# Kernel tuning notes

Hardware: AMD Instinct MI355X
Metric: run time of the kernel (lower is better)

Reference implementation:

```python
import jax, jax.numpy as jnp
import numpy as np

N = 8192
D = 512  # token_length
EPS = 1e-12  # torch F.normalize default eps


def setup_inputs() -> dict:
    key = jax.random.key(0)
    ks = jax.random.split(key, 7)
    scale = 1.0 / np.sqrt(D)  # torch Linear init range ~ U(-1/sqrt(D), 1/sqrt(D))
    def lin(k):
        kw, kb = jax.random.split(k)
        W = jax.random.uniform(kw, (D, D), jnp.float32, -scale, scale)
        b = jax.random.uniform(kb, (D,), jnp.float32, -scale, scale)
        return W, b
    Wq, bq = lin(ks[0])
    Wk, bk = lin(ks[1])
    Wv, bv = lin(ks[2])
    x = jax.random.normal(ks[3], (N, D), jnp.float32)
    return {"x": x, "Wq": Wq, "bq": bq, "Wk": Wk, "bk": bk, "Wv": Wv, "bv": bv}


def reference(x, Wq, bq, Wk, bk, Wv, bv):
    # torch Linear: y = x @ W^T + b
    q = x @ Wq.T + bq            # [N, D]
    k = x @ Wk.T + bk            # [N, D]
    v = x @ Wv.T + bv            # [N, D]
    s = q @ k.T                  # [N, N] scores
    # F.normalize(s): L2-normalize each row (dim=1), eps=1e-12
    norm = jnp.sqrt(jnp.sum(s * s, axis=1, keepdims=True))
    w = s / jnp.maximum(norm, EPS)
    return w @ v                 # [N, D]
```

## Files before the change

### kernel.cpp

```cpp
#include <hip/hip_runtime.h>
#include <hip/hip_bf16.h>
#include <stdint.h>

#define NTOK 8192
#define DIM  512
#define QKVW 1536

typedef __attribute__((ext_vector_type(8))) short bf16x8;
typedef __attribute__((ext_vector_type(4))) float f32x4;

static __device__ __forceinline__ unsigned short f2b(float f) {
    union { float f; unsigned int u; } v; v.f = f;
    unsigned int r = v.u + 0x7fffu + ((v.u >> 16) & 1u);
    return (unsigned short)(r >> 16);
}

static __device__ __forceinline__ float b2f(unsigned short u) {
    union { unsigned int i; float f; } v; v.i = ((unsigned int)u) << 16;
    return v.f;
}

static __device__ __forceinline__ void gld_lds16(const void* g, void* l) {
    __builtin_amdgcn_global_load_lds(
        (__attribute__((address_space(1))) void*)(uintptr_t)g,
        (__attribute__((address_space(3))) void*)(uintptr_t)l,
        16, 0, 0);
}

#define SBAR() do { __builtin_amdgcn_sched_barrier(0); __builtin_amdgcn_s_barrier(); __builtin_amdgcn_sched_barrier(0); } while (0)
#define VMW0() do { __builtin_amdgcn_sched_barrier(0); asm volatile("s_waitcnt vmcnt(0)" ::: "memory"); __builtin_amdgcn_sched_barrier(0); } while (0)
#define LGKM0() do { __builtin_amdgcn_sched_barrier(0); asm volatile("s_waitcnt lgkmcnt(0)" ::: "memory"); __builtin_amdgcn_sched_barrier(0); } while (0)


__global__ void f2b_kernel(const float* __restrict__ src, unsigned short* __restrict__ dst, int n4) {
    int i = blockIdx.x * blockDim.x + threadIdx.x;
    if (i < n4) {
        float4 f = ((const float4*)src)[i];
        ushort4 o;
        o.x = f2b(f.x); o.y = f2b(f.y); o.z = f2b(f.z); o.w = f2b(f.w);
        ((ushort4*)dst)[i] = o;
    }
}

__global__ void f2b_w3(const float* __restrict__ w0, const float* __restrict__ w1,
                       const float* __restrict__ w2, unsigned short* __restrict__ dst) {
    int which = blockIdx.y;
    const float* src = (which == 0) ? w0 : (which == 1) ? w1 : w2;
    int i = blockIdx.x * 256 + threadIdx.x;
    float4 f = ((const float4*)src)[i];
    ushort4 o;
    o.x = f2b(f.x); o.y = f2b(f.y); o.z = f2b(f.z); o.w = f2b(f.w);
    ((ushort4*)(dst + (size_t)which * 262144))[i] = o;
}

__global__ void bias_concat(const float* __restrict__ bq, const float* __restrict__ bk,
                            const float* __restrict__ bv, float* __restrict__ bc) {
    int i = blockIdx.x * blockDim.x + threadIdx.x;
    if (i < 512)       bc[i] = bq[i];
    else if (i < 1024) bc[i] = bk[i - 512];
    else if (i < 1536) bc[i] = bv[i - 1024];
}

template <int CH, int NT>
__global__ __launch_bounds__(256, 4) void gemm_qkv2(
    const unsigned short* __restrict__ A, int lda,
    const unsigned short* __restrict__ B, int ldb,
    unsigned short* __restrict__ Qb,
    unsigned short* __restrict__ KVt,
    const float* __restrict__ bias) {

    __shared__ __align__(16) char lds[32768];

    const int t = threadIdx.x;
    const int l = t & 63, w = t >> 6;
    const int wr = w >> 1, wc = w & 1;

    const int gx = gridDim.x;
    const int nbm = gridDim.y >> 3;
    const int bid = blockIdx.y * gx + blockIdx.x;
    const int xcd = bid & 7, qq = bid >> 3;
    const int win = nbm * CH;
    const int grp = qq / win, rr = qq % win;
    const int bm = xcd * nbm + rr / CH;
    const int bn = grp * CH + rr % CH;

    const int c0 = w * 128 + l;
    const int c1 = c0 + 64;
    const int r0 = c0 >> 2, r1 = c1 >> 2;
    const int col0 = (((c0 & 3) ^ ((c0 >> 3) & 3)) << 3);
    const int col1 = (((c1 & 3) ^ ((c1 >> 3) & 3)) << 3);
    const unsigned short* gA0 = A + (size_t)(bm * 128 + r0) * lda + col0;
    const unsigned short* gA1 = A + (size_t)(bm * 128 + r1) * lda + col1;
    const unsigned short* gB0 = B + (size_t)(bn * 128 + r0) * ldb + col0;
    const unsigned short* gB1 = B + (size_t)(bn * 128 + r1) * ldb + col1;

    auto STAGE = [&](int buf, int tt) {
        char* d = lds + buf * 16384 + w * 2048;
        const int o = tt * 32;
        gld_lds16(gA0 + o, d);
        gld_lds16(gA1 + o, d + 1024);
        gld_lds16(gB0 + o, d + 8192);
        gld_lds16(gB1 + o, d + 8192 + 1024);
    };

    f32x4 acc[4][4] = {};

    const int lr = l & 15, Q = l >> 4;
    const int sw = ((Q ^ ((lr >> 1) & 3)) << 4);
    const int lrA = (wr * 64 + lr) * 64 + sw;
    const int lrB = 8192 + (wc * 64 + lr) * 64 + sw;

    STAGE(0, 0);
    VMW0();
    SBAR();

    #pragma unroll
    for (int tt = 0; tt < NT; ++tt) {
        const int cur = tt & 1;
        const bool more = (tt + 1 < NT);
        if (more) STAGE(cur ^ 1, tt + 1);
        __builtin_amdgcn_sched_barrier(0);

        const char* lb = lds + cur * 16384;
        bf16x8 af[4], bf[4];
        #pragma unroll
        for (int m = 0; m < 4; ++m) af[m] = *(const bf16x8*)(lb + lrA + m * 1024);
        #pragma unroll
        for (int n = 0; n < 4; ++n) bf[n] = *(const bf16x8*)(lb + lrB + n * 1024);

        __builtin_amdgcn_s_setprio(1);
        #pragma unroll
        for (int m = 0; m < 4; ++m)
            #pragma unroll
            for (int n = 0; n < 4; ++n)
                acc[m][n] = __builtin_amdgcn_mfma_f32_16x16x32_bf16(af[m], bf[n], acc[m][n], 0, 0, 0);
        __builtin_amdgcn_s_setprio(0);

        if (more) {
            VMW0();
            SBAR();
        }
    }

    const int rbase = bm * 128 + wr * 64;
    const int cbase = bn * 128 + wc * 64;
    const int g4 = Q * 4;

    if (bn < 4) {
        #pragma unroll
        for (int m = 0; m < 4; ++m)
            #pragma unroll
            for (int n = 0; n < 4; ++n)
                #pragma unroll
                for (int j = 0; j < 4; ++j) {
                    int rrow = rbase + m * 16 + g4 + j;
                    int ccol = cbase + n * 16 + lr;
                    Qb[(size_t)rrow * 512 + ccol] = f2b(acc[m][n][j] + bias[ccol]);
                }
    } else {
        SBAR();
        unsigned short* wt = (unsigned short*)(lds + w * 8192);
        #pragma unroll
        for (int p = 0; p < 2; ++p) {
            #pragma unroll
            for (int m = 0; m < 4; ++m)
                #pragma unroll
                for (int q2 = 0; q2 < 2; ++q2) {
                    int n = 2 * p + q2;
                    int cloc = q2 * 16 + lr;
                    int ccol = cbase + n * 16 + lr;
                    unsigned short s0 = f2b(acc[m][n][0] + bias[ccol]);
                    unsigned short s1 = f2b(acc[m][n][1] + bias[ccol]);
                    unsigned short s2 = f2b(acc[m][n][2] + bias[ccol]);
                    unsigned short s3 = f2b(acc[m][n][3] + bias[ccol]);
                    uint2 v;
                    v.x = (unsigned int)s0 | ((unsigned int)s1 << 16);
                    v.y = (unsigned int)s2 | ((unsigned int)s3 << 16);
                    *(uint2*)(wt + cloc * 72 + m * 16 + g4) = v;
                }
            LGKM0();
            const int kvb = cbase - 512 + 32 * p;
            #pragma unroll
            for (int cc = 0; cc < 8; ++cc) {
                int cloc = cc * 4 + Q;
                uint2 v = *(const uint2*)(wt + cloc * 72 + lr * 4);
                *(uint2*)&KVt[(size_t)(kvb + cloc) * NTOK + rbase + lr * 4] = v;
            }
            if (p == 0) LGKM0();
        }
    }
}

template <int EPI, int CH, int NT>
__global__ __launch_bounds__(256, 4) void gemm7(
    const unsigned short* __restrict__ A, int lda,
    const unsigned short* __restrict__ B, int ldb,
    void* __restrict__ Cout, int ldc,
    const unsigned short* __restrict__ Qb,
    float* __restrict__ nrm) {

    __shared__ __align__(16) char lds[32768];

    const int t = threadIdx.x;
    const int l = t & 63, w = t >> 6;
    const int wr = w >> 1, wc = w & 1;

    int bm, bn;
    if constexpr (CH == 0) {
        bm = blockIdx.y; bn = blockIdx.x;
    } else {
        const int gx = gridDim.x;
        const int nbm = gridDim.y >> 3;
        const int bid = blockIdx.y * gx + blockIdx.x;
        const int xcd = bid & 7, qq = bid >> 3;
        const int win = nbm * CH;
        const int grp = qq / win, rr = qq % win;
        bm = xcd * nbm + rr / CH;
        bn = grp * CH + rr % CH;
    }

    const int kt0 = blockIdx.z * (NT * 32);

    const int c0 = w * 128 + l;
    const int c1 = c0 + 64;
    const int r0 = c0 >> 2, r1 = c1 >> 2;
    const int col0 = (((c0 & 3) ^ ((c0 >> 3) & 3)) << 3);
    const int col1 = (((c1 & 3) ^ ((c1 >> 3) & 3)) << 3);
    const unsigned short* gA0 = A + (size_t)(bm * 128 + r0) * lda + kt0 + col0;
    const unsigned short* gA1 = A + (size_t)(bm * 128 + r1) * lda + kt0 + col1;
    const unsigned short* gB0 = B + (size_t)(bn * 128 + r0) * ldb + kt0 + col0;
    const unsigned short* gB1 = B + (size_t)(bn * 128 + r1) * ldb + kt0 + col1;

    auto STAGE = [&](int buf, int tt) {
        char* d = lds + buf * 16384 + w * 2048;
        const int o = tt * 32;
        gld_lds16(gA0 + o, d);
        gld_lds16(gA1 + o, d + 1024);
        gld_lds16(gB0 + o, d + 8192);
        gld_lds16(gB1 + o, d + 8192 + 1024);
    };

    f32x4 acc[4][4] = {};

    const int lr = l & 15, Q = l >> 4;
    const int sw = ((Q ^ ((lr >> 1) & 3)) << 4);
    const int lrA = (wr * 64 + lr) * 64 + sw;
    const int lrB = 8192 + (wc * 64 + lr) * 64 + sw;

    STAGE(0, 0);
    VMW0();
    SBAR();

    #pragma unroll
    for (int tt = 0; tt < NT; ++tt) {
        const int cur = tt & 1;
        const bool more = (tt + 1 < NT);
        if (more) STAGE(cur ^ 1, tt + 1);
        __builtin_amdgcn_sched_barrier(0);

        const char* lb = lds + cur * 16384;
        bf16x8 af[4], bf[4];
        #pragma unroll
        for (int m = 0; m < 4; ++m) af[m] = *(const bf16x8*)(lb + lrA + m * 1024);
        #pragma unroll
        for (int n = 0; n < 4; ++n) bf[n] = *(const bf16x8*)(lb + lrB + n * 1024);

        __builtin_amdgcn_s_setprio(1);
        #pragma unroll
        for (int m = 0; m < 4; ++m)
            #pragma unroll
            for (int n = 0; n < 4; ++n)
                acc[m][n] = __builtin_amdgcn_mfma_f32_16x16x32_bf16(af[m], bf[n], acc[m][n], 0, 0, 0);
        __builtin_amdgcn_s_setprio(0);

        if (more) {
            VMW0();
            SBAR();
        }
    }

    const int rbase = bm * 128 + wr * 64;
    const int cbase = bn * 128 + wc * 64;
    const int g4 = Q * 4;

    if constexpr (EPI == 2) {
        unsigned short* C = (unsigned short*)Cout + (size_t)blockIdx.z * 524288;
        #pragma unroll
        for (int m = 0; m < 4; ++m)
            #pragma unroll
            for (int n = 0; n < 4; ++n)
                #pragma unroll
                for (int j = 0; j < 4; ++j) {
                    int rrow = rbase + m * 16 + g4 + j;
                    int ccol = cbase + n * 16 + lr;
                    C[(size_t)rrow * ldc + ccol] = f2b(acc[m][n][j]);
                }
    } else {
        if (bn < 4) {
            #pragma unroll
            for (int m = 0; m < 4; ++m)
                #pragma unroll
                for (int j = 0; j < 4; ++j) {
                    int rrow = rbase + m * 16 + g4 + j;
                    float p = 0.f;
                    #pragma unroll
                    for (int n = 0; n < 4; ++n) {
                        float qv = b2f(Qb[(size_t)rrow * 512 + cbase + n * 16 + lr]);
                        p += acc[m][n][j] * qv;
                    }
                    p += __shfl_xor(p, 1);
                    p += __shfl_xor(p, 2);
                    p += __shfl_xor(p, 4);
                    p += __shfl_xor(p, 8);
                    if (lr == 0) atomicAdd(&nrm[rrow], p);
                }
        } else {
            unsigned short* C = (unsigned short*)Cout;
            #pragma unroll
            for (int m = 0; m < 4; ++m)
                #pragma unroll
                for (int n = 0; n < 4; ++n)
                    #pragma unroll
                    for (int j = 0; j < 4; ++j) {
                        int rrow = rbase + m * 16 + g4 + j;
                        int ccol = cbase - 512 + n * 16 + lr;
                        C[(size_t)rrow * ldc + ccol] = f2b(acc[m][n][j]);
                    }
        }
    }
}

__global__ void reduce_gh(const unsigned short* __restrict__ part, unsigned short* __restrict__ ght) {
    int i = blockIdx.x * 256 + threadIdx.x;
    float4 s = {0.f, 0.f, 0.f, 0.f};
    #pragma unroll
    for (int z = 0; z < 16; ++z) {
        ushort4 v = ((const ushort4*)(part + (size_t)z * 524288))[i];
        s.x += b2f(v.x); s.y += b2f(v.y); s.z += b2f(v.z); s.w += b2f(v.w);
    }
    ushort4 o;
    o.x = f2b(s.x); o.y = f2b(s.y); o.z = f2b(s.z); o.w = f2b(s.w);
    ((ushort4*)ght)[i] = o;
}

__global__ void final_norm(const unsigned short* __restrict__ U16, const float* __restrict__ nrm,
                           float* __restrict__ out) {
    int i = blockIdx.x * 256 + threadIdx.x;
    ushort4 u = ((const ushort4*)U16)[i];
    int row = i >> 7;
    float inv = 1.0f / fmaxf(sqrtf(nrm[row]), 1e-12f);
    float4 o;
    o.x = b2f(u.x) * inv; o.y = b2f(u.y) * inv; o.z = b2f(u.z) * inv; o.w = b2f(u.w) * inv;
    ((float4*)out)[i] = o;
}

extern "C" void kernel_launch(void* const* d_in, const int* in_sizes, int n_in,
                              void* d_out, int out_size, void* d_ws, size_t ws_size,
                              hipStream_t stream) {
    const float* x  = (const float*)d_in[0];
    const float* Wq = (const float*)d_in[1];
    const float* bq = (const float*)d_in[2];
    const float* Wk = (const float*)d_in[3];
    const float* bk = (const float*)d_in[4];
    const float* Wv = (const float*)d_in[5];
    const float* bv = (const float*)d_in[6];
    float* out = (float*)d_out;

    char* ws = (char*)d_ws;
    size_t off = 0;
    auto alloc = [&](size_t bytes) -> void* {
        void* p = ws + off;
        off = (off + bytes + 255) & ~(size_t)255;
        return p;
    };

    unsigned short* xb   = (unsigned short*)alloc((size_t)NTOK * DIM * 2);
    unsigned short* Wb   = (unsigned short*)alloc((size_t)QKVW * DIM * 2);
    float*          bc   = (float*)alloc(QKVW * 4);
    unsigned short* Qb   = (unsigned short*)alloc((size_t)NTOK * DIM * 2);
    unsigned short* KVt  = (unsigned short*)alloc((size_t)1024 * NTOK * 2);
    unsigned short* GHp  = (unsigned short*)alloc((size_t)16 * 1024 * 512 * 2);
    unsigned short* GHt  = (unsigned short*)alloc((size_t)1024 * 512 * 2);
    unsigned short* U16  = (unsigned short*)alloc((size_t)NTOK * DIM * 2);
    float*          nrm  = (float*)alloc(NTOK * 4);

    f2b_kernel<<<(NTOK * DIM / 4 + 255) / 256, 256, 0, stream>>>(x, xb, NTOK * DIM / 4);
    f2b_w3<<<dim3(DIM * DIM / 4 / 256, 3), 256, 0, stream>>>(Wq, Wk, Wv, Wb);
    bias_concat<<<6, 256, 0, stream>>>(bq, bk, bv, bc);
    hipMemsetAsync(nrm, 0, NTOK * 4, stream);

    gemm_qkv2<12, 16><<<dim3(QKVW / 128, NTOK / 128), 256, 0, stream>>>(
        xb, DIM, Wb, DIM, Qb, KVt, bc);

    gemm7<2, 0, 16><<<dim3(512 / 128, 1024 / 128, 16), 256, 0, stream>>>(
        KVt, NTOK, KVt, NTOK, GHp, 512, nullptr, nullptr);

    reduce_gh<<<512, 256, 0, stream>>>(GHp, GHt);

    gemm7<4, 8, 16><<<dim3(1024 / 128, NTOK / 128), 256, 0, stream>>>(
        Qb, 512, GHt, 512, U16, DIM, Qb, nrm);

    final_norm<<<NTOK * DIM / 4 / 256, 256, 0, stream>>>(U16, nrm, out);
}
```

Before: 80.50 us.

## Deepen GEMM K-tile to 64 and fuse prep kernels into one launch

The three GEMM kernels now stage K-tiles of 64 instead of 32. LDS per block doubles to 64KB with a matching 8-way XOR swizzle, and the loop runs half as many iterations, so there are half as many barriers and wait points per unit of work. The conversion, bias-concat and nrm-zeroing kernels plus the memset are merged into a single prep launch to cut launch overhead. In exchange, occupancy falls (launch bounds go from 4 to 2 blocks per CU, with larger LDS) and each wave holds more fragment registers.

```diff
diff --git a/kernel.cpp b/kernel.cpp
--- a/kernel.cpp
+++ b/kernel.cpp
@@ -31,45 +31,51 @@
 #define VMW0() do { __builtin_amdgcn_sched_barrier(0); asm volatile("s_waitcnt vmcnt(0)" ::: "memory"); __builtin_amdgcn_sched_barrier(0); } while (0)
 #define LGKM0() do { __builtin_amdgcn_sched_barrier(0); asm volatile("s_waitcnt lgkmcnt(0)" ::: "memory"); __builtin_amdgcn_sched_barrier(0); } while (0)
 
-
-__global__ void f2b_kernel(const float* __restrict__ src, unsigned short* __restrict__ dst, int n4) {
-    int i = blockIdx.x * blockDim.x + threadIdx.x;
-    if (i < n4) {
+__global__ void prep(const float* __restrict__ x,
+                     const float* __restrict__ Wq, const float* __restrict__ Wk,
+                     const float* __restrict__ Wv,
+                     const float* __restrict__ bq, const float* __restrict__ bk,
+                     const float* __restrict__ bv,
+                     unsigned short* __restrict__ xb, unsigned short* __restrict__ Wb,
+                     float* __restrict__ bc, float* __restrict__ nrm) {
+    int b = blockIdx.x, t = threadIdx.x;
+    if (b < 4096) {
+        int i = b * 256 + t;
+        float4 f = ((const float4*)x)[i];
+        ushort4 o;
+        o.x = f2b(f.x); o.y = f2b(f.y); o.z = f2b(f.z); o.w = f2b(f.w);
+        ((ushort4*)xb)[i] = o;
+    } else if (b < 4864) {
+        int bb = b - 4096;
+        int which = bb >> 8;
+        const float* src = (which == 0) ? Wq : (which == 1) ? Wk : Wv;
+        int i = (bb & 255) * 256 + t;
         float4 f = ((const float4*)src)[i];
         ushort4 o;
         o.x = f2b(f.x); o.y = f2b(f.y); o.z = f2b(f.z); o.w = f2b(f.w);
-        ((ushort4*)dst)[i] = o;
-    }
-}
-
-__global__ void f2b_w3(const float* __restrict__ w0, const float* __restrict__ w1,
-                       const float* __restrict__ w2, unsigned short* __restrict__ dst) {
-    int which = blockIdx.y;
-    const float* src = (which == 0) ? w0 : (which == 1) ? w1 : w2;
-    int i = blockIdx.x * 256 + threadIdx.x;
-    float4 f = ((const float4*)src)[i];
-    ushort4 o;
-    o.x = f2b(f.x); o.y = f2b(f.y); o.z = f2b(f.z); o.w = f2b(f.w);
-    ((ushort4*)(dst + (size_t)which * 262144))[i] = o;
-}
-
-__global__ void bias_concat(const float* __restrict__ bq, const float* __restrict__ bk,
-                            const float* __restrict__ bv, float* __restrict__ bc) {
-    int i = blockIdx.x * blockDim.x + threadIdx.x;
-    if (i < 512)       bc[i] = bq[i];
-    else if (i < 1024) bc[i] = bk[i - 512];
-    else if (i < 1536) bc[i] = bv[i - 1024];
-}
+        ((ushort4*)(Wb + (size_t)which * 262144))[i] = o;
+    } else if (b < 4870) {
+        int i = (b - 4864) * 256 + t;
+        if (i < 512)       bc[i] = bq[i];
+        else if (i < 1024) bc[i] = bk[i - 512];
+        else               bc[i] = bv[i - 1024];
+    } else {
+        int i = (b - 4870) * 256 + t;
+        float4 z = {0.f, 0.f, 0.f, 0.f};
+        ((float4*)nrm)[i] = z;
+    }
+}
+
 
 template <int CH, int NT>
-__global__ __launch_bounds__(256, 4) void gemm_qkv2(
+__global__ __launch_bounds__(256, 2) void gemm_qkv3(
     const unsigned short* __restrict__ A, int lda,
     const unsigned short* __restrict__ B, int ldb,
     unsigned short* __restrict__ Qb,
     unsigned short* __restrict__ KVt,
     const float* __restrict__ bias) {
 
-    __shared__ __align__(16) char lds[32768];
+    __shared__ __align__(16) char lds[65536];
 
     const int t = threadIdx.x;
     const int l = t & 63, w = t >> 6;
@@ -84,31 +90,34 @@
     const int bm = xcd * nbm + rr / CH;
     const int bn = grp * CH + rr % CH;
 
-    const int c0 = w * 128 + l;
-    const int c1 = c0 + 64;
-    const int r0 = c0 >> 2, r1 = c1 >> 2;
-    const int col0 = (((c0 & 3) ^ ((c0 >> 3) & 3)) << 3);
-    const int col1 = (((c1 & 3) ^ ((c1 >> 3) & 3)) << 3);
-    const unsigned short* gA0 = A + (size_t)(bm * 128 + r0) * lda + col0;
-    const unsigned short* gA1 = A + (size_t)(bm * 128 + r1) * lda + col1;
-    const unsigned short* gB0 = B + (size_t)(bn * 128 + r0) * ldb + col0;
-    const unsigned short* gB1 = B + (size_t)(bn * 128 + r1) * ldb + col1;
+    const unsigned short* sA[4];
+    const unsigned short* sB[4];
+    #pragma unroll
+    for (int i = 0; i < 4; ++i) {
+        int c = i * 256 + t;
+        int row = c >> 3;
+        int p = (c & 7) ^ ((row >> 1) & 7);
+        sA[i] = A + (size_t)(bm * 128 + row) * lda + p * 8;
+        sB[i] = B + (size_t)(bn * 128 + row) * ldb + p * 8;
+    }
 
     auto STAGE = [&](int buf, int tt) {
-        char* d = lds + buf * 16384 + w * 2048;
-        const int o = tt * 32;
-        gld_lds16(gA0 + o, d);
-        gld_lds16(gA1 + o, d + 1024);
-        gld_lds16(gB0 + o, d + 8192);
-        gld_lds16(gB1 + o, d + 8192 + 1024);
+        char* d = lds + buf * 32768 + w * 1024;
+        const int o = tt * 64;
+        #pragma unroll
+        for (int i = 0; i < 4; ++i) {
+            gld_lds16(sA[i] + o, d + i * 4096);
+            gld_lds16(sB[i] + o, d + 16384 + i * 4096);
+        }
     };
 
     f32x4 acc[4][4] = {};
 
     const int lr = l & 15, Q = l >> 4;
-    const int sw = ((Q ^ ((lr >> 1) & 3)) << 4);
-    const int lrA = (wr * 64 + lr) * 64 + sw;
-    const int lrB = 8192 + (wc * 64 + lr) * 64 + sw;
+    const int g = (lr >> 1) & 7;
+    const int sw0 = ((Q ^ g) << 4), sw1 = (((Q + 4) ^ g) << 4);
+    const int lrA = (wr * 64 + lr) * 128;
+    const int lrB = 16384 + (wc * 64 + lr) * 128;
 
     STAGE(0, 0);
     VMW0();
@@ -121,19 +130,27 @@
         if (more) STAGE(cur ^ 1, tt + 1);
         __builtin_amdgcn_sched_barrier(0);
 
-        const char* lb = lds + cur * 16384;
-        bf16x8 af[4], bf[4];
-        #pragma unroll
-        for (int m = 0; m < 4; ++m) af[m] = *(const bf16x8*)(lb + lrA + m * 1024);
-        #pragma unroll
-        for (int n = 0; n < 4; ++n) bf[n] = *(const bf16x8*)(lb + lrB + n * 1024);
+        const char* lb = lds + cur * 32768;
+        bf16x8 af[4][2], bf[4][2];
+        #pragma unroll
+        for (int m = 0; m < 4; ++m) {
+            af[m][0] = *(const bf16x8*)(lb + lrA + m * 2048 + sw0);
+            af[m][1] = *(const bf16x8*)(lb + lrA + m * 2048 + sw1);
+        }
+        #pragma unroll
+        for (int n = 0; n < 4; ++n) {
+            bf[n][0] = *(const bf16x8*)(lb + lrB + n * 2048 + sw0);
+            bf[n][1] = *(const bf16x8*)(lb + lrB + n * 2048 + sw1);
+        }
 
         __builtin_amdgcn_s_setprio(1);
         #pragma unroll
         for (int m = 0; m < 4; ++m)
             #pragma unroll
-            for (int n = 0; n < 4; ++n)
-                acc[m][n] = __builtin_amdgcn_mfma_f32_16x16x32_bf16(af[m], bf[n], acc[m][n], 0, 0, 0);
+            for (int n = 0; n < 4; ++n) {
+                acc[m][n] = __builtin_amdgcn_mfma_f32_16x16x32_bf16(af[m][0], bf[n][0], acc[m][n], 0, 0, 0);
+                acc[m][n] = __builtin_amdgcn_mfma_f32_16x16x32_bf16(af[m][1], bf[n][1], acc[m][n], 0, 0, 0);
+            }
         __builtin_amdgcn_s_setprio(0);
 
         if (more) {
@@ -192,14 +209,14 @@
 }
 
 template <int EPI, int CH, int NT>
-__global__ __launch_bounds__(256, 4) void gemm7(
+__global__ __launch_bounds__(256, 2) void gemm8b(
     const unsigned short* __restrict__ A, int lda,
     const unsigned short* __restrict__ B, int ldb,
     void* __restrict__ Cout, int ldc,
     const unsigned short* __restrict__ Qb,
     float* __restrict__ nrm) {
 
-    __shared__ __align__(16) char lds[32768];
+    __shared__ __align__(16) char lds[65536];
 
     const int t = threadIdx.x;
     const int l = t & 63, w = t >> 6;
@@ -219,33 +236,36 @@
         bn = grp * CH + rr % CH;
     }
 
-    const int kt0 = blockIdx.z * (NT * 32);
-
-    const int c0 = w * 128 + l;
-    const int c1 = c0 + 64;
-    const int r0 = c0 >> 2, r1 = c1 >> 2;
-    const int col0 = (((c0 & 3) ^ ((c0 >> 3) & 3)) << 3);
-    const int col1 = (((c1 & 3) ^ ((c1 >> 3) & 3)) << 3);
-    const unsigned short* gA0 = A + (size_t)(bm * 128 + r0) * lda + kt0 + col0;
-    const unsigned short* gA1 = A + (size_t)(bm * 128 + r1) * lda + kt0 + col1;
-    const unsigned short* gB0 = B + (size_t)(bn * 128 + r0) * ldb + kt0 + col0;
-    const unsigned short* gB1 = B + (size_t)(bn * 128 + r1) * ldb + kt0 + col1;
+    const int kt0 = blockIdx.z * (NT * 64);
+
+    const unsigned short* sA[4];
+    const unsigned short* sB[4];
+    #pragma unroll
+    for (int i = 0; i < 4; ++i) {
+        int c = i * 256 + t;
+        int row = c >> 3;
+        int p = (c & 7) ^ ((row >> 1) & 7);
+        sA[i] = A + (size_t)(bm * 128 + row) * lda + kt0 + p * 8;
+        sB[i] = B + (size_t)(bn * 128 + row) * ldb + kt0 + p * 8;
+    }
 
     auto STAGE = [&](int buf, int tt) {
-        char* d = lds + buf * 16384 + w * 2048;
-        const int o = tt * 32;
-        gld_lds16(gA0 + o, d);
-        gld_lds16(gA1 + o, d + 1024);
-        gld_lds16(gB0 + o, d + 8192);
-        gld_lds16(gB1 + o, d + 8192 + 1024);
+        char* d = lds + buf * 32768 + w * 1024;
+        const int o = tt * 64;
+        #pragma unroll
+        for (int i = 0; i < 4; ++i) {
+            gld_lds16(sA[i] + o, d + i * 4096);
+            gld_lds16(sB[i] + o, d + 16384 + i * 4096);
+        }
     };
 
     f32x4 acc[4][4] = {};
 
     const int lr = l & 15, Q = l >> 4;
-    const int sw = ((Q ^ ((lr >> 1) & 3)) << 4);
-    const int lrA = (wr * 64 + lr) * 64 + sw;
-    const int lrB = 8192 + (wc * 64 + lr) * 64 + sw;
+    const int g = (lr >> 1) & 7;
+    const int sw0 = ((Q ^ g) << 4), sw1 = (((Q + 4) ^ g) << 4);
+    const int lrA = (wr * 64 + lr) * 128;
+    const int lrB = 16384 + (wc * 64 + lr) * 128;
 
     STAGE(0, 0);
     VMW0();
@@ -258,19 +278,27 @@
         if (more) STAGE(cur ^ 1, tt + 1);
         __builtin_amdgcn_sched_barrier(0);
 
-        const char* lb = lds + cur * 16384;
-        bf16x8 af[4], bf[4];
-        #pragma unroll
-        for (int m = 0; m < 4; ++m) af[m] = *(const bf16x8*)(lb + lrA + m * 1024);
-        #pragma unroll
-        for (int n = 0; n < 4; ++n) bf[n] = *(const bf16x8*)(lb + lrB + n * 1024);
+        const char* lb = lds + cur * 32768;
+        bf16x8 af[4][2], bf[4][2];
+        #pragma unroll
+        for (int m = 0; m < 4; ++m) {
+            af[m][0] = *(const bf16x8*)(lb + lrA + m * 2048 + sw0);
+            af[m][1] = *(const bf16x8*)(lb + lrA + m * 2048 + sw1);
+        }
+        #pragma unroll
+        for (int n = 0; n < 4; ++n) {
+            bf[n][0] = *(const bf16x8*)(lb + lrB + n * 2048 + sw0);
+            bf[n][1] = *(const bf16x8*)(lb + lrB + n * 2048 + sw1);
+        }
 
         __builtin_amdgcn_s_setprio(1);
         #pragma unroll
         for (int m = 0; m < 4; ++m)
             #pragma unroll
-            for (int n = 0; n < 4; ++n)
-                acc[m][n] = __builtin_amdgcn_mfma_f32_16x16x32_bf16(af[m], bf[n], acc[m][n], 0, 0, 0);
+            for (int n = 0; n < 4; ++n) {
+                acc[m][n] = __builtin_amdgcn_mfma_f32_16x16x32_bf16(af[m][0], bf[n][0], acc[m][n], 0, 0, 0);
+                acc[m][n] = __builtin_amdgcn_mfma_f32_16x16x32_bf16(af[m][1], bf[n][1], acc[m][n], 0, 0, 0);
+            }
         __builtin_amdgcn_s_setprio(0);
 
         if (more) {
@@ -384,20 +412,17 @@
     unsigned short* U16  = (unsigned short*)alloc((size_t)NTOK * DIM * 2);
     float*          nrm  = (float*)alloc(NTOK * 4);
 
-    f2b_kernel<<<(NTOK * DIM / 4 + 255) / 256, 256, 0, stream>>>(x, xb, NTOK * DIM / 4);
-    f2b_w3<<<dim3(DIM * DIM / 4 / 256, 3), 256, 0, stream>>>(Wq, Wk, Wv, Wb);
-    bias_concat<<<6, 256, 0, stream>>>(bq, bk, bv, bc);
-    hipMemsetAsync(nrm, 0, NTOK * 4, stream);
-
-    gemm_qkv2<12, 16><<<dim3(QKVW / 128, NTOK / 128), 256, 0, stream>>>(
+    prep<<<4878, 256, 0, stream>>>(x, Wq, Wk, Wv, bq, bk, bv, xb, Wb, bc, nrm);
+
+    gemm_qkv3<12, 8><<<dim3(QKVW / 128, NTOK / 128), 256, 0, stream>>>(
         xb, DIM, Wb, DIM, Qb, KVt, bc);
 
-    gemm7<2, 0, 16><<<dim3(512 / 128, 1024 / 128, 16), 256, 0, stream>>>(
+    gemm8b<2, 0, 8><<<dim3(512 / 128, 1024 / 128, 16), 256, 0, stream>>>(
         KVt, NTOK, KVt, NTOK, GHp, 512, nullptr, nullptr);
 
     reduce_gh<<<512, 256, 0, stream>>>(GHp, GHt);
 
-    gemm7<4, 8, 16><<<dim3(1024 / 128, NTOK / 128), 256, 0, stream>>>(
+    gemm8b<4, 8, 8><<<dim3(1024 / 128, NTOK / 128), 256, 0, stream>>>(
         Qb, 512, GHt, 512, U16, DIM, Qb, nrm);
 
     final_norm<<<NTOK * DIM / 4 / 256, 256, 0, stream>>>(U16, nrm, out);
```

New measurement: 71.51 us, median of 2. 11.2% less time.
